# Kernel tuning notes

Hardware: AMD Instinct MI355X
Metric: run time of the kernel (lower is better)

## Reference

```python
import jax, jax.numpy as jnp
import numpy as np

N = 50000        # nodes
E = 400000       # edges per relation graph
IN_DIM = 64
HID = 128
OUT_DIM = 2
NSEL = 4096
EPS = 0.3        # residual scale
SLOPE = 0.3      # LeakyReLU negative slope


def _leaky(x):
    return jnp.where(x >= 0, x, SLOPE * x)


def _deg_norm(dst):
    # FAGCN-style d = in_degree^{-1/2}; 0 for isolated nodes
    deg = jax.ops.segment_sum(jnp.ones(dst.shape[0], jnp.float32), dst, num_segments=N)
    return jnp.where(deg > 0, jax.lax.rsqrt(jnp.maximum(deg, 1.0)), 0.0)


def _gnn_layer(hf, src, dst, d, gw, gb):
    # gate(concat[h_dst, h_src]) computed as per-node projections then edge gather
    D = hf.shape[1]
    s_dst = hf @ gw[:D]   # [N]
    s_src = hf @ gw[D:]   # [N]
    a = jnp.tanh(s_dst[dst] + s_src[src] + gb)        # [E]
    e = a * d[dst] * d[src]                            # [E]
    msg = hf[src] * e[:, None]                         # [E, D]
    return jax.ops.segment_sum(msg, dst, num_segments=N)


def setup_inputs() -> dict:
    key = jax.random.key(0)
    ks = iter(jax.random.split(key, 48))
    def nrm(shape, scale=0.05):
        return jax.random.normal(next(ks), shape, jnp.float32) * scale
    inp = {}
    inp["h"] = jax.random.normal(next(ks), (N, IN_DIM), jnp.float32)
    for i in (1, 2, 3):
        inp[f"src{i}"] = jax.random.randint(next(ks), (E,), 0, N)
        inp[f"dst{i}"] = jax.random.randint(next(ks), (E,), 0, N)
    inp["nodes"] = jax.random.randint(next(ks), (NSEL,), 0, N)
    inp["t1_w"] = nrm((HID, IN_DIM)); inp["t1_b"] = jnp.zeros((HID,), jnp.float32)
    for i in (1, 2, 3):
        inp[f"gate1_{i}_w"] = nrm((2 * HID,)); inp[f"gate1_{i}_b"] = jnp.zeros((), jnp.float32)
        inp[f"gate2_{i}_w"] = nrm((6 * HID,)); inp[f"gate2_{i}_b"] = jnp.zeros((), jnp.float32)
        inp[f"hw1_{i}"] = nrm((HID, HID))
        inp[f"hw2_{i}"] = nrm((3 * HID, HID))
    inp["t2_w"] = nrm((64, 7 * HID + IN_DIM)); inp["t2_b"] = jnp.zeros((64,), jnp.float32)
    inp["t3_w"] = nrm((OUT_DIM, 64)); inp["t3_b"] = jnp.zeros((OUT_DIM,), jnp.float32)
    return inp


def reference(h, src1, dst1, src2, dst2, src3, dst3, nodes,
              t1_w, t1_b,
              gate1_1_w, gate1_1_b, gate1_2_w, gate1_2_b, gate1_3_w, gate1_3_b,
              gate2_1_w, gate2_1_b, gate2_2_w, gate2_2_b, gate2_3_w, gate2_3_b,
              hw1_1, hw1_2, hw1_3, hw2_1, hw2_2, hw2_3,
              t2_w, t2_b, t3_w, t3_b):
    d1, d2, d3 = _deg_norm(dst1), _deg_norm(dst2), _deg_norm(dst3)
    raw0 = h
    raw1 = _leaky(h @ t1_w.T + t1_b)   # [N, HID] (dropout=identity in eval)
    h1_1 = _leaky((EPS * raw1 + _gnn_layer(raw1, src1, dst1, d1, gate1_1_w, gate1_1_b)) @ hw1_1)
    h1_2 = _leaky((EPS * raw1 + _gnn_layer(raw1, src2, dst2, d2, gate1_2_w, gate1_2_b)) @ hw1_2)
    h1_3 = _leaky((EPS * raw1 + _gnn_layer(raw1, src3, dst3, d3, gate1_3_w, gate1_3_b)) @ hw1_3)
    raw2 = jnp.concatenate([h1_1, h1_2, h1_3], axis=1)   # [N, 3*HID]
    h2_1 = _leaky((EPS * raw2 + _gnn_layer(raw2, src1, dst1, d1, gate2_1_w, gate2_1_b)) @ hw2_1)
    h2_2 = _leaky((EPS * raw2 + _gnn_layer(raw2, src2, dst2, d2, gate2_2_w, gate2_2_b)) @ hw2_2)
    h2_3 = _leaky((EPS * raw2 + _gnn_layer(raw2, src3, dst3, d3, gate2_3_w, gate2_3_b)) @ hw2_3)
    hf = jnp.concatenate([h2_1, h2_2, h2_3, raw0, raw1, raw2], axis=1)  # [N, 7*HID+IN_DIM]
    nf = hf[nodes]                                       # [NSEL, 7*HID+IN_DIM]
    s = _leaky(nf @ t2_w.T + t2_b)
    return s @ t3_w.T + t3_b                             # [NSEL, OUT_DIM]
```

## Files before the change

kernel.cpp:

```cpp
#include <hip/hip_runtime.h>
#include <hip/hip_bf16.h>

#define NN 50000
#define NE 400000
#define IND 64
#define HID 128
#define H3 384
#define FDIM 960
#define NSEL 4096
#define EPSF 0.3f
#define SLOPEF 0.3f
#define NBK 196
#define BCAP 4096
#define EPB 4096
#define NOEDGE 0xFFFFFFFFu

typedef __attribute__((ext_vector_type(8))) short bfrag;
typedef __attribute__((ext_vector_type(4))) float f4;
typedef __attribute__((ext_vector_type(8))) unsigned short us8;

__device__ __forceinline__ float leaky1(float v){ return v>=0.f? v : SLOPEF*v; }
__device__ __forceinline__ float b2f(unsigned short u){
  return __uint_as_float(((unsigned)u)<<16);
}
__device__ __forceinline__ unsigned short f2b(float v){
  __hip_bfloat16 b = __float2bfloat16(v);
  return *(unsigned short*)&b;
}

__global__ __launch_bounds__(256) void k_bfill4(
    const int* __restrict__ s0,const int* __restrict__ d0,
    const int* __restrict__ s1,const int* __restrict__ d1,
    const int* __restrict__ s2,const int* __restrict__ d2,
    int* __restrict__ bcnt, unsigned int* __restrict__ pairbuf)
{
  __shared__ unsigned int lbuf[EPB];
  __shared__ int hist[256];
  __shared__ int lbase[256];
  __shared__ int lcur[256];
  __shared__ int gbase[NBK];
  __shared__ int wsum[4];
  const int r = blockIdx.y;
  const int* S = (r==0)?s0:((r==1)?s1:s2);
  const int* D = (r==0)?d0:((r==1)?d1:d2);
  const int e0 = blockIdx.x*EPB;
  const int t = threadIdx.x;
  hist[t] = 0; lcur[t] = 0;
  __syncthreads();

  unsigned int pv[16];
  #pragma unroll
  for (int j=0;j<4;j++){
    int e = e0 + (j*256 + t)*4;
    if (e < NE){
      int4 sv = *(const int4*)&S[e];
      int4 dv = *(const int4*)&D[e];
      pv[j*4+0] = ((unsigned)dv.x<<16)|(unsigned)sv.x;
      pv[j*4+1] = ((unsigned)dv.y<<16)|(unsigned)sv.y;
      pv[j*4+2] = ((unsigned)dv.z<<16)|(unsigned)sv.z;
      pv[j*4+3] = ((unsigned)dv.w<<16)|(unsigned)sv.w;
    } else {
      pv[j*4+0]=NOEDGE; pv[j*4+1]=NOEDGE; pv[j*4+2]=NOEDGE; pv[j*4+3]=NOEDGE;
    }
  }
  #pragma unroll
  for (int i=0;i<16;i++){
    if (pv[i] != NOEDGE) atomicAdd(&hist[pv[i]>>24], 1);
  }
  __syncthreads();
  {
    int hv = hist[t];
    int lane = t & 63, wid = t >> 6;
    int x = hv;
    #pragma unroll
    for (int d=1; d<64; d<<=1){ int y=__shfl_up(x,(unsigned)d); if(lane>=d) x+=y; }
    if (lane==63) wsum[wid]=x;
    __syncthreads();
    int wpre = 0;
    if (wid>0) wpre += wsum[0];
    if (wid>1) wpre += wsum[1];
    if (wid>2) wpre += wsum[2];
    lbase[t] = wpre + x - hv;
    if (t < NBK){
      int hh = hist[t];
      gbase[t] = (hh>0) ? atomicAdd(&bcnt[r*NBK+t], hh) : 0;
    }
  }
  __syncthreads();
  #pragma unroll
  for (int i=0;i<16;i++){
    if (pv[i] != NOEDGE){
      int b = (int)(pv[i] >> 24);
      int pos = lbase[b] + atomicAdd(&lcur[b], 1);
      lbuf[pos] = pv[i];
    }
  }
  __syncthreads();
  int tot = min(NE - e0, EPB);
  for (int idx = t; idx < tot; idx += 256){
    unsigned int v = lbuf[idx];
    int b = (int)(v >> 24);
    pairbuf[((size_t)(r*NBK + b))*BCAP + gbase[b] + (idx - lbase[b])] = v;
  }
}

__global__ __launch_bounds__(256) void k_bsort4(
    const unsigned int* __restrict__ pairbuf,
    const int* __restrict__ bcnt,
    int* __restrict__ off, float* __restrict__ dnv,
    unsigned short* __restrict__ csrc)
{
  __shared__ unsigned short lout[BCAP];
  __shared__ int hist[256];
  __shared__ int excl[256];
  __shared__ int cur[256];
  __shared__ int red[256];
  __shared__ int wsum[4];
  const int r = blockIdx.y, b = blockIdx.x;
  const int nb0 = b << 8;
  const int t = threadIdx.x;
  red[t] = (t < b) ? bcnt[r*NBK + t] : 0;
  hist[t] = 0; cur[t] = 0;
  __syncthreads();
  #pragma unroll
  for (int sdv=128; sdv>0; sdv>>=1){
    if (t < sdv) red[t] += red[t+sdv];
    __syncthreads();
  }
  const int bbase = red[0];
  const int cnt = bcnt[r*NBK + b];
  const unsigned int* pb = pairbuf + ((size_t)(r*NBK + b))*BCAP;
  unsigned int pv[16];
  #pragma unroll
  for (int j=0;j<16;j++){
    int e = j*256 + t;
    pv[j] = (e < cnt) ? pb[e] : NOEDGE;
    if (pv[j] != NOEDGE) atomicAdd(&hist[(int)(pv[j]>>16) - nb0], 1);
  }
  __syncthreads();
  {
    int hv = hist[t];
    int lane = t & 63, wid = t >> 6;
    int x = hv;
    #pragma unroll
    for (int d=1; d<64; d<<=1){ int y=__shfl_up(x,(unsigned)d); if(lane>=d) x+=y; }
    if (lane==63) wsum[wid]=x;
    __syncthreads();
    int wpre = 0;
    if (wid>0) wpre += wsum[0];
    if (wid>1) wpre += wsum[1];
    if (wid>2) wpre += wsum[2];
    excl[t] = wpre + x - hv;
  }
  __syncthreads();
  int nidx = nb0 + t;
  if (nidx < NN){
    off[r*(NN+1) + nidx] = bbase + excl[t];
    int g = hist[t];
    dnv[r*NN + nidx] = (g>0) ? rsqrtf((float)g) : 0.f;
  }
  if (b == NBK-1 && t == 0) off[r*(NN+1) + NN] = bbase + cnt;
  #pragma unroll
  for (int j=0;j<16;j++){
    if (pv[j] != NOEDGE){
      int pn = (int)(pv[j] >> 16) - nb0;
      int slot = atomicAdd(&cur[pn], 1);
      lout[excl[pn] + slot] = (unsigned short)(pv[j] & 0xffffu);
    }
  }
  __syncthreads();
  unsigned short* op = csrc + (size_t)r*NE + bbase;
  for (int idx = t; idx < cnt; idx += 256) op[idx] = lout[idx];
}

__global__ void k_wprep2(const float* __restrict__ t1w,
    const float* __restrict__ hw1_0, const float* __restrict__ hw1_1, const float* __restrict__ hw1_2,
    const float* __restrict__ hw2_0, const float* __restrict__ hw2_1, const float* __restrict__ hw2_2,
    const float* __restrict__ t2w, const float* __restrict__ h,
    unsigned short* __restrict__ wt1, unsigned short* __restrict__ w1t,
    unsigned short* __restrict__ w2t, unsigned short* __restrict__ wt2,
    unsigned short* __restrict__ hb){
  int t = blockIdx.x*256 + threadIdx.x;
  if (t < 8192){
    wt1[t] = f2b(t1w[t]);
  } else if (t < 57344){
    int e = t - 8192;
    int r = e / 16384, q = e - r*16384;
    int n = q >> 7, k = q & 127;
    const float* W = (r==0)?hw1_0:((r==1)?hw1_1:hw1_2);
    w1t[e] = f2b(W[k*HID + n]);
  } else if (t < 204800){
    int e = t - 57344;
    int r = e / 49152, q = e - r*49152;
    int n = q / H3, k = q - n*H3;
    const float* W = (r==0)?hw2_0:((r==1)?hw2_1:hw2_2);
    w2t[e] = f2b(W[k*HID + n]);
  } else if (t < 266240){
    int e = t - 204800;
    wt2[e] = f2b(t2w[e]);
  } else if (t < 666240){
    int q = t - 266240;
    const float4 a = ((const float4*)h)[q*2];
    const float4 b = ((const float4*)h)[q*2+1];
    us8 o;
    o[0]=f2b(a.x); o[1]=f2b(a.y); o[2]=f2b(a.z); o[3]=f2b(a.w);
    o[4]=f2b(b.x); o[5]=f2b(b.y); o[6]=f2b(b.z); o[7]=f2b(b.w);
    *(us8*)&hb[q*8] = o;
  }
}

__global__ __launch_bounds__(256) void k_mfma_t1(
    const unsigned short* __restrict__ Ab, const unsigned short* __restrict__ W,
    const float* __restrict__ bias, unsigned short* __restrict__ Cb)
{
  __shared__ short As[64][72];
  __shared__ short Bs[128][72];
  const int tid = threadIdx.x;
  const int bm = blockIdx.x*64;

  for (int q = tid; q < 64*8; q += 256){
    int row = q >> 3, c8 = q & 7;
    int grow = bm + row; grow = (grow < NN) ? grow : (NN-1);
    *(us8*)&As[row][c8*8] = *(const us8*)&Ab[(size_t)grow*IND + c8*8];
  }
  for (int q = tid; q < 128*8; q += 256){
    int n = q >> 3, c8 = q & 7;
    *(us8*)&Bs[n][c8*8] = *(const us8*)&W[n*IND + c8*8];
  }
  __syncthreads();

  const int wid = tid >> 6, lane = tid & 63;
  const int wrow = (wid & 1)*32, wcol = (wid >> 1)*64;
  const int fr = lane & 15, fq = lane >> 4;
  f4 acc[2][4];
  #pragma unroll
  for (int mi=0;mi<2;mi++)
    #pragma unroll
    for (int ni=0;ni<4;ni++) acc[mi][ni] = (f4){0.f,0.f,0.f,0.f};

  #pragma unroll
  for (int ks=0; ks<2; ks++){
    int kb = ks*32 + fq*8;
    bfrag a[2], b[4];
    #pragma unroll
    for (int mi=0;mi<2;mi++) a[mi] = *(const bfrag*)&As[wrow + mi*16 + fr][kb];
    #pragma unroll
    for (int ni=0;ni<4;ni++) b[ni] = *(const bfrag*)&Bs[wcol + ni*16 + fr][kb];
    #pragma unroll
    for (int mi=0;mi<2;mi++)
      #pragma unroll
      for (int ni=0;ni<4;ni++)
        acc[mi][ni] = __builtin_amdgcn_mfma_f32_16x16x32_bf16(a[mi], b[ni], acc[mi][ni], 0, 0, 0);
  }

  #pragma unroll
  for (int mi=0;mi<2;mi++){
    int row0 = bm + wrow + mi*16 + fq*4;
    #pragma unroll
    for (int j=0;j<4;j++){
      int row = row0 + j;
      if (row < NN){
        #pragma unroll
        for (int ni=0;ni<4;ni++){
          int col = wcol + ni*16 + fr;
          Cb[(size_t)row*HID + col] = f2b(leaky1(acc[mi][ni][j] + bias[col]));
        }
      }
    }
  }
}

__global__ __launch_bounds__(256) void k_mfma128(
    const unsigned short* __restrict__ Abf, const unsigned short* __restrict__ Wt,
    unsigned short* __restrict__ Cb, int M)
{
  __shared__ short As[64][136];
  __shared__ short Bs[128][136];
  const int r = blockIdx.y;
  const unsigned short* Ar = Abf + (size_t)r*M*HID;
  const unsigned short* W  = Wt + (size_t)r*HID*HID;
  const int tid = threadIdx.x;
  const int bm = blockIdx.x*64;

  for (int q = tid; q < 64*16; q += 256){
    int row = q >> 4, c8 = q & 15;
    int grow = bm + row; grow = (grow < M) ? grow : (M-1);
    *(us8*)&As[row][c8*8] = *(const us8*)&Ar[(size_t)grow*HID + c8*8];
  }
  for (int q = tid; q < 128*16; q += 256){
    int n = q >> 4, c8 = q & 15;
    *(us8*)&Bs[n][c8*8] = *(const us8*)&W[n*HID + c8*8];
  }
  __syncthreads();

  const int wid = tid >> 6, lane = tid & 63;
  const int wrow = (wid & 1)*32, wcol = (wid >> 1)*64;
  const int fr = lane & 15, fq = lane >> 4;
  f4 acc[2][4];
  #pragma unroll
  for (int mi=0;mi<2;mi++)
    #pragma unroll
    for (int ni=0;ni<4;ni++) acc[mi][ni] = (f4){0.f,0.f,0.f,0.f};

  #pragma unroll
  for (int ks=0; ks<4; ks++){
    int kb = ks*32 + fq*8;
    bfrag a[2], b[4];
    #pragma unroll
    for (int mi=0;mi<2;mi++) a[mi] = *(const bfrag*)&As[wrow + mi*16 + fr][kb];
    #pragma unroll
    for (int ni=0;ni<4;ni++) b[ni] = *(const bfrag*)&Bs[wcol + ni*16 + fr][kb];
    #pragma unroll
    for (int mi=0;mi<2;mi++)
      #pragma unroll
      for (int ni=0;ni<4;ni++)
        acc[mi][ni] = __builtin_amdgcn_mfma_f32_16x16x32_bf16(a[mi], b[ni], acc[mi][ni], 0, 0, 0);
  }

  const int coff = r*HID;
  #pragma unroll
  for (int mi=0;mi<2;mi++){
    int row0 = bm + wrow + mi*16 + fq*4;
    #pragma unroll
    for (int j=0;j<4;j++){
      int row = row0 + j;
      if (row < M){
        #pragma unroll
        for (int ni=0;ni<4;ni++){
          Cb[(size_t)row*H3 + coff + wcol + ni*16 + fr] = f2b(leaky1(acc[mi][ni][j]));
        }
      }
    }
  }
}

__global__ __launch_bounds__(256) void k_mfma384(
    const unsigned short* __restrict__ Abf, const unsigned short* __restrict__ Wt,
    unsigned short* __restrict__ nfb)
{
  __shared__ short As[32][72];
  __shared__ short Bs[128][72];
  const int r = blockIdx.y;
  const unsigned short* Ar = Abf + (size_t)r*NSEL*H3;
  const unsigned short* W  = Wt + (size_t)r*HID*H3;
  const int tid = threadIdx.x;
  const int bm = blockIdx.x*32;
  const int wid = tid >> 6, lane = tid & 63;
  const int fr = lane & 15, fq = lane >> 4;
  f4 acc[2][2];
  #pragma unroll
  for (int mi=0;mi<2;mi++)
    #pragma unroll
    for (int ni=0;ni<2;ni++) acc[mi][ni] = (f4){0.f,0.f,0.f,0.f};

  for (int kc=0; kc<6; kc++){
    for (int q = tid; q < 32*8; q += 256){
      int row = q >> 3, c8 = q & 7;
      *(us8*)&As[row][c8*8] = *(const us8*)&Ar[(size_t)(bm+row)*H3 + kc*64 + c8*8];
    }
    for (int q = tid; q < 128*8; q += 256){
      int n = q >> 3, c8 = q & 7;
      *(us8*)&Bs[n][c8*8] = *(const us8*)&W[(size_t)n*H3 + kc*64 + c8*8];
    }
    __syncthreads();
    #pragma unroll
    for (int ks=0; ks<2; ks++){
      int kb = ks*32 + fq*8;
      bfrag a[2], b[2];
      #pragma unroll
      for (int mi=0;mi<2;mi++) a[mi] = *(const bfrag*)&As[mi*16 + fr][kb];
      #pragma unroll
      for (int ni=0;ni<2;ni++) b[ni] = *(const bfrag*)&Bs[wid*32 + ni*16 + fr][kb];
      #pragma unroll
      for (int mi=0;mi<2;mi++)
        #pragma unroll
        for (int ni=0;ni<2;ni++)
          acc[mi][ni] = __builtin_amdgcn_mfma_f32_16x16x32_bf16(a[mi], b[ni], acc[mi][ni], 0, 0, 0);
    }
    __syncthreads();
  }

  #pragma unroll
  for (int mi=0;mi<2;mi++){
    int row0 = bm + mi*16 + fq*4;
    #pragma unroll
    for (int j=0;j<4;j++){
      int i = row0 + j;
      #pragma unroll
      for (int ni=0;ni<2;ni++){
        int col = wid*32 + ni*16 + fr;
        nfb[(size_t)i*FDIM + r*HID + col] = f2b(leaky1(acc[mi][ni][j]));
      }
    }
  }
}

__global__ __launch_bounds__(256) void k_mfma_t2(
    const unsigned short* __restrict__ Abf, const unsigned short* __restrict__ W,
    float* __restrict__ sbuf)
{
  __shared__ short As[32][72];
  __shared__ short Bs[64][72];
  const int tid = threadIdx.x;
  const int bm = blockIdx.x*32;
  const int wid = tid >> 6, lane = tid & 63;
  const int fr = lane & 15, fq = lane >> 4;
  f4 acc[2];
  acc[0] = (f4){0.f,0.f,0.f,0.f};
  acc[1] = (f4){0.f,0.f,0.f,0.f};

  for (int kc=0; kc<15; kc++){
    for (int q = tid; q < 32*8; q += 256){
      int row = q >> 3, c8 = q & 7;
      *(us8*)&As[row][c8*8] = *(const us8*)&Abf[(size_t)(bm+row)*FDIM + kc*64 + c8*8];
    }
    for (int q = tid; q < 64*8; q += 256){
      int n = q >> 3, c8 = q & 7;
      *(us8*)&Bs[n][c8*8] = *(const us8*)&W[(size_t)n*FDIM + kc*64 + c8*8];
    }
    __syncthreads();
    #pragma unroll
    for (int ks=0; ks<2; ks++){
      int kb = ks*32 + fq*8;
      bfrag a[2], b;
      a[0] = *(const bfrag*)&As[fr][kb];
      a[1] = *(const bfrag*)&As[16 + fr][kb];
      b = *(const bfrag*)&Bs[wid*16 + fr][kb];
      acc[0] = __builtin_amdgcn_mfma_f32_16x16x32_bf16(a[0], b, acc[0], 0, 0, 0);
      acc[1] = __builtin_amdgcn_mfma_f32_16x16x32_bf16(a[1], b, acc[1], 0, 0, 0);
    }
    __syncthreads();
  }

  #pragma unroll
  for (int mi=0;mi<2;mi++){
    int row0 = bm + mi*16 + fq*4;
    #pragma unroll
    for (int j=0;j<4;j++){
      sbuf[(size_t)(row0+j)*64 + wid*16 + fr] = acc[mi][j];
    }
  }
}

__global__ __launch_bounds__(256) void k_final_wave(
    const float* __restrict__ sbuf, const float* __restrict__ t2b,
    const float* __restrict__ t3w, const float* __restrict__ t3b,
    float* __restrict__ outp)
{
  int w = (blockIdx.x*256 + threadIdx.x) >> 6;
  int j = threadIdx.x & 63;
  if (w >= NSEL) return;
  float v = leaky1(sbuf[(size_t)w*64 + j] + t2b[j]);
  float a0 = v*t3w[j], a1 = v*t3w[64+j];
  #pragma unroll
  for (int sft=32;sft>0;sft>>=1){
    a0 += __shfl_down(a0,(unsigned)sft);
    a1 += __shfl_down(a1,(unsigned)sft);
  }
  if (j==0){
    outp[2*w+0] = a0 + t3b[0];
    outp[2*w+1] = a1 + t3b[1];
  }
}

template<int D>
__global__ __launch_bounds__(256) void k_scores_g(const unsigned short* __restrict__ X,
    const float* __restrict__ g0, const float* __restrict__ g1, const float* __restrict__ g2,
    float* __restrict__ sd, float* __restrict__ ss){
  const int tid = threadIdx.x;
  const int p = tid & 15;
  const int n = blockIdx.x*16 + (tid >> 4);
  const unsigned short* x = X + (size_t)n*D;
  float a0=0,a1=0,a2=0,a3=0,a4=0,a5=0;
  #pragma unroll
  for (int it=0; it<D/128; it++){
    int k = it*128 + p*8;
    us8 u = *(const us8*)&x[k];
    #pragma unroll
    for (int e=0;e<8;e++){
      float v = b2f(u[e]);
      a0 = fmaf(v, g0[k+e],   a0);  a1 = fmaf(v, g0[D+k+e], a1);
      a2 = fmaf(v, g1[k+e],   a2);  a3 = fmaf(v, g1[D+k+e], a3);
      a4 = fmaf(v, g2[k+e],   a4);  a5 = fmaf(v, g2[D+k+e], a5);
    }
  }
  #pragma unroll
  for (int s=8;s>0;s>>=1){
    a0 += __shfl_xor(a0,(unsigned)s); a1 += __shfl_xor(a1,(unsigned)s);
    a2 += __shfl_xor(a2,(unsigned)s); a3 += __shfl_xor(a3,(unsigned)s);
    a4 += __shfl_xor(a4,(unsigned)s); a5 += __shfl_xor(a5,(unsigned)s);
  }
  if (p==0){
    sd[0*NN+n]=a0; ss[0*NN+n]=a1;
    sd[1*NN+n]=a2; ss[1*NN+n]=a3;
    sd[2*NN+n]=a4; ss[2*NN+n]=a5;
  }
}

__global__ __launch_bounds__(256) void k_gather_f3z(
    const unsigned short* __restrict__ Xb,
    const int* __restrict__ off, const unsigned short* __restrict__ csrc,
    const float* __restrict__ sd, const float* __restrict__ ss,
    const float* __restrict__ dnv,
    const float* __restrict__ gb0, const float* __restrict__ gb1, const float* __restrict__ gb2,
    unsigned short* __restrict__ outp){
  const int tid = threadIdx.x;
  const int lane = tid & 63;
  const int wg = lane >> 4;
  const int p  = lane & 15;
  const int n = blockIdx.x*16 + (tid >> 4);
  us8 rv = *(const us8*)&Xb[(size_t)n*HID + p*8];
  int p0a[3], p1a[3];
  #pragma unroll
  for (int r=0;r<3;r++){
    p0a[r] = off[r*(NN+1) + n];
    p1a[r] = off[r*(NN+1) + n + 1];
  }
  float resid[8];
  #pragma unroll
  for (int i=0;i<8;i++) resid[i] = EPSF * b2f(rv[i]);

  for (int r=0;r<3;r++){
    const unsigned short* csr = csrc + (size_t)r*NE;
    const float* ssr = ss + r*NN;
    const float* dnr = dnv + r*NN;
    float gbv = ((r==0)?gb0:((r==1)?gb1:gb2))[0];
    float sd_n = sd[r*NN + n], dn_n = dnr[n];
    float acc[8];
    #pragma unroll
    for (int i=0;i<8;i++) acc[i] = resid[i];
    int p0 = p0a[r], p1 = p1a[r];
    for (int pc=p0; pc<p1; pc+=16){
      int m = min(16, p1-pc);
      int s = 0; float c = 0.f;
      if (p < m){
        s = csr[pc+p];
        c = tanhf(sd_n + ssr[s] + gbv) * dn_n * dnr[s];
      }
      int   sj = __shfl(s, wg*16);
      float cj = __shfl(c, wg*16);
      us8 v = *(const us8*)&Xb[(size_t)sj*HID + p*8];
      for (int j=1;j<=m;j++){
        us8 vn; float cn = 0.f;
        if (j < m){
          int sn = __shfl(s, wg*16+j);
          cn = __shfl(c, wg*16+j);
          vn = *(const us8*)&Xb[(size_t)sn*HID + p*8];
        }
        #pragma unroll
        for (int i=0;i<8;i++) acc[i] = fmaf(cj, b2f(v[i]), acc[i]);
        v = vn; cj = cn;
      }
    }
    us8 o;
    #pragma unroll
    for (int i=0;i<8;i++) o[i] = f2b(acc[i]);
    *(us8*)&outp[((size_t)r*NN + n)*HID + p*8] = o;
  }
}

__global__ __launch_bounds__(256) void k_gather_sel3w2(const unsigned short* __restrict__ Xb,
    const int* __restrict__ nodes,
    const int* __restrict__ off, const unsigned short* __restrict__ csrc,
    const float* __restrict__ sd, const float* __restrict__ ss,
    const float* __restrict__ dnv,
    const float* __restrict__ gb0, const float* __restrict__ gb1, const float* __restrict__ gb2,
    unsigned short* __restrict__ outp){
  const int tid = threadIdx.x;
  const int lane = tid & 63;
  const int wg = lane >> 4;
  const int p  = lane & 15;
  const int i = blockIdx.x*16 + (tid >> 4);
  const int r = blockIdx.y;
  const int n = nodes[i];
  const int* offr = off + r*(NN+1);
  const unsigned short* csr = csrc + (size_t)r*NE;
  const float* ssr = ss + r*NN;
  const float* dnr = dnv + r*NN;
  float gbv = ((r==0)?gb0:((r==1)?gb1:gb2))[0];
  float sd_n = sd[r*NN + n], dn_n = dnr[n];
  float acc[3][8];
  #pragma unroll
  for (int cc=0;cc<3;cc++)
    #pragma unroll
    for (int q=0;q<8;q++) acc[cc][q]=0.f;
  int p0 = offr[n], p1 = offr[n+1];
  for (int pc=p0; pc<p1; pc+=16){
    int m = min(16, p1-pc);
    int s = 0; float c = 0.f;
    if (p < m){
      s = csr[pc+p];
      c = tanhf(sd_n + ssr[s] + gbv) * dn_n * dnr[s];
    }
    int   sj = __shfl(s, wg*16);
    float cj = __shfl(c, wg*16);
    const unsigned short* row = &Xb[(size_t)sj*H3];
    us8 v0 = *(const us8*)&row[0*HID + p*8];
    us8 v1 = *(const us8*)&row[1*HID + p*8];
    us8 v2 = *(const us8*)&row[2*HID + p*8];
    for (int j=1;j<=m;j++){
      us8 n0, n1, n2; float cn = 0.f;
      if (j < m){
        int sn = __shfl(s, wg*16+j);
        cn = __shfl(c, wg*16+j);
        const unsigned short* rw = &Xb[(size_t)sn*H3];
        n0 = *(const us8*)&rw[0*HID + p*8];
        n1 = *(const us8*)&rw[1*HID + p*8];
        n2 = *(const us8*)&rw[2*HID + p*8];
      }
      #pragma unroll
      for (int q=0;q<8;q++){
        acc[0][q] = fmaf(cj, b2f(v0[q]), acc[0][q]);
        acc[1][q] = fmaf(cj, b2f(v1[q]), acc[1][q]);
        acc[2][q] = fmaf(cj, b2f(v2[q]), acc[2][q]);
      }
      v0 = n0; v1 = n1; v2 = n2; cj = cn;
    }
  }
  const unsigned short* xrow = &Xb[(size_t)n*H3];
  unsigned short* orow = &outp[((size_t)r*NSEL + i)*H3];
  #pragma unroll
  for (int cc=0;cc<3;cc++){
    us8 v = *(const us8*)&xrow[cc*HID + p*8];
    us8 o;
    #pragma unroll
    for (int q=0;q<8;q++) o[q] = f2b(fmaf(EPSF, b2f(v[q]), acc[cc][q]));
    *(us8*)&orow[cc*HID + p*8] = o;
  }
}

__global__ __launch_bounds__(256) void k_nf_fillb(const unsigned short* __restrict__ hb,
    const unsigned short* __restrict__ raw1b, const unsigned short* __restrict__ raw2b,
    const int* __restrict__ nodes, unsigned short* __restrict__ nfb){
  int t = blockIdx.x*256 + threadIdx.x;
  if (t >= NSEL*72) return;
  int i = t/72, c = t - i*72;
  int n = nodes[i];
  us8 v; int col;
  if (c < 8)       { v = *(const us8*)&hb[(size_t)n*IND + c*8];           col = 384 + c*8; }
  else if (c < 24) { int q=c-8;  v = *(const us8*)&raw1b[(size_t)n*HID + q*8]; col = 448 + q*8; }
  else             { int q=c-24; v = *(const us8*)&raw2b[(size_t)n*H3  + q*8]; col = 576 + q*8; }
  *(us8*)&nfb[(size_t)i*FDIM + col] = v;
}

extern "C" void kernel_launch(void* const* d_in, const int* in_sizes, int n_in,
                              void* d_out, int out_size, void* d_ws, size_t ws_size,
                              hipStream_t stream){
  if (n_in < 32) return;
  const float* h = (const float*)d_in[0];
  const int* src[3] = {(const int*)d_in[1], (const int*)d_in[3], (const int*)d_in[5]};
  const int* dst[3] = {(const int*)d_in[2], (const int*)d_in[4], (const int*)d_in[6]};
  const int* nodes = (const int*)d_in[7];
  const float* t1w = (const float*)d_in[8];
  const float* t1b = (const float*)d_in[9];

  bool dictOrder = (in_sizes[12] == 768);
  const float *g1w[3],*g1b[3],*g2w[3],*g2b[3],*hw1[3],*hw2[3];
  for (int r=0;r<3;r++){
    if (dictOrder){
      int base = 10 + r*6;
      g1w[r]=(const float*)d_in[base+0]; g1b[r]=(const float*)d_in[base+1];
      g2w[r]=(const float*)d_in[base+2]; g2b[r]=(const float*)d_in[base+3];
      hw1[r]=(const float*)d_in[base+4]; hw2[r]=(const float*)d_in[base+5];
    } else {
      g1w[r]=(const float*)d_in[10+2*r]; g1b[r]=(const float*)d_in[11+2*r];
      g2w[r]=(const float*)d_in[16+2*r]; g2b[r]=(const float*)d_in[17+2*r];
      hw1[r]=(const float*)d_in[22+r];   hw2[r]=(const float*)d_in[25+r];
    }
  }
  const float* t2w = (const float*)d_in[28];
  const float* t2b = (const float*)d_in[29];
  const float* t3w = (const float*)d_in[30];
  const float* t3b = (const float*)d_in[31];
  float* outp = (float*)d_out;

  char* w = (char*)d_ws;
  auto carve = [&](size_t bytes)->void*{
    void* p = (void*)w;
    w += ((bytes + 255) & ~size_t(255));
    return p;
  };
  int*   bcnt = (int*)  carve((size_t)1024*4);
  int*   off  = (int*)  carve((size_t)3*(NN+1)*4);
  float* dnv  = (float*)carve((size_t)3*NN*4);
  unsigned short* csrc = (unsigned short*)carve((size_t)3*NE*2);
  float* sd1  = (float*)carve((size_t)3*NN*4);
  float* ss1  = (float*)carve((size_t)3*NN*4);
  float* sd2  = (float*)carve((size_t)3*NN*4);
  float* ss2  = (float*)carve((size_t)3*NN*4);
  unsigned short* wt1 = (unsigned short*)carve((size_t)HID*IND*2);
  unsigned short* w1t = (unsigned short*)carve((size_t)3*HID*HID*2);
  unsigned short* w2t = (unsigned short*)carve((size_t)3*HID*H3*2);
  unsigned short* wt2 = (unsigned short*)carve((size_t)64*FDIM*2);
  unsigned short* hb  = (unsigned short*)carve((size_t)NN*IND*2);
  unsigned short* raw1b = (unsigned short*)carve((size_t)NN*HID*2);
  unsigned short* raw2b = (unsigned short*)carve((size_t)NN*H3*2);
  size_t ubytes = (size_t)3*NN*HID*2;
  float* ureg = (float*)carve(ubytes);
  unsigned int* pairbuf = (unsigned int*)ureg;
  unsigned short* pre1b = (unsigned short*)ureg;
  unsigned short* pre2b = (unsigned short*)ureg;
  float* sbuf = (float*)((char*)ureg + (size_t)16*1024*1024);
  unsigned short* nfb = (unsigned short*)carve((size_t)NSEL*FDIM*2);

  hipMemsetAsync(bcnt, 0, (size_t)1024*4, stream);
  k_bfill4<<<dim3((NE+EPB-1)/EPB, 3), 256, 0, stream>>>(
      src[0],dst[0],src[1],dst[1],src[2],dst[2], bcnt, pairbuf);
  k_bsort4<<<dim3(NBK,3), 256, 0, stream>>>(pairbuf, bcnt, off, dnv, csrc);

  k_wprep2<<<(666240+255)/256, 256, 0, stream>>>(
      t1w, hw1[0], hw1[1], hw1[2], hw2[0], hw2[1], hw2[2], t2w, h,
      wt1, w1t, w2t, wt2, hb);

  k_mfma_t1<<<(NN+63)/64, 256, 0, stream>>>(hb, wt1, t1b, raw1b);

  k_scores_g<HID><<<NN/16, 256, 0, stream>>>(raw1b, g1w[0], g1w[1], g1w[2], sd1, ss1);

  k_gather_f3z<<<NN/16, 256, 0, stream>>>(raw1b, off, csrc,
      sd1, ss1, dnv, g1b[0], g1b[1], g1b[2], pre1b);
  k_mfma128<<<dim3((NN+63)/64, 3), 256, 0, stream>>>(pre1b, w1t, raw2b, NN);

  k_scores_g<H3><<<NN/16, 256, 0, stream>>>(raw2b, g2w[0], g2w[1], g2w[2], sd2, ss2);

  k_gather_sel3w2<<<dim3(NSEL/16, 3), 256, 0, stream>>>(raw2b, nodes, off, csrc,
      sd2, ss2, dnv, g2b[0], g2b[1], g2b[2], pre2b);

  k_mfma384<<<dim3(NSEL/32, 3), 256, 0, stream>>>(pre2b, w2t, nfb);

  k_nf_fillb<<<(NSEL*72+255)/256, 256, 0, stream>>>(hb, raw1b, raw2b, nodes, nfb);

  k_mfma_t2<<<NSEL/32, 256, 0, stream>>>(nfb, wt2, sbuf);
  k_final_wave<<<(NSEL*64+255)/256, 256, 0, stream>>>(sbuf, t2b, t3w, t3b, outp);
}
```

Measured before the change: 197.0 us.

## Merge independent kernels into combined launches to cut launch count

Independent kernels are merged into shared launches by splitting on block index: edge bucket fill with weight/feature bf16 prep, bucket sort with the t1 MFMA GEMM, and the hw2 GEMM with the node-feature gather. The t2 GEMM and final projection are also fused through shared memory, removing the sbuf round trip. This reduces kernel launch overhead and inter-kernel gaps. The cost is larger shared-memory footprints and mixed block types within a launch.

Result: faster. 186.1 us (-5.6%).

```diff
diff --git a/kernel.cpp b/kernel.cpp
--- a/kernel.cpp
+++ b/kernel.cpp
@@ -14,6 +14,7 @@
 #define BCAP 4096
 #define EPB 4096
 #define NOEDGE 0xFFFFFFFFu
+#define NBF 98
 
 typedef __attribute__((ext_vector_type(8))) short bfrag;
 typedef __attribute__((ext_vector_type(4))) float f4;
@@ -28,242 +29,239 @@
   return *(unsigned short*)&b;
 }
 
-__global__ __launch_bounds__(256) void k_bfill4(
+__global__ __launch_bounds__(256) void k_fill_prep(
     const int* __restrict__ s0,const int* __restrict__ d0,
     const int* __restrict__ s1,const int* __restrict__ d1,
     const int* __restrict__ s2,const int* __restrict__ d2,
-    int* __restrict__ bcnt, unsigned int* __restrict__ pairbuf)
+    int* __restrict__ bcnt, unsigned int* __restrict__ pairbuf,
+    const float* __restrict__ t1w,
+    const float* __restrict__ hw1_0, const float* __restrict__ hw1_1, const float* __restrict__ hw1_2,
+    const float* __restrict__ hw2_0, const float* __restrict__ hw2_1, const float* __restrict__ hw2_2,
+    const float* __restrict__ t2w, const float* __restrict__ h,
+    unsigned short* __restrict__ wt1, unsigned short* __restrict__ w1t,
+    unsigned short* __restrict__ w2t, unsigned short* __restrict__ wt2,
+    unsigned short* __restrict__ hb)
 {
-  __shared__ unsigned int lbuf[EPB];
+  __shared__ __align__(16) unsigned int lbuf[EPB];
   __shared__ int hist[256];
   __shared__ int lbase[256];
   __shared__ int lcur[256];
   __shared__ int gbase[NBK];
   __shared__ int wsum[4];
-  const int r = blockIdx.y;
-  const int* S = (r==0)?s0:((r==1)?s1:s2);
-  const int* D = (r==0)?d0:((r==1)?d1:d2);
-  const int e0 = blockIdx.x*EPB;
   const int t = threadIdx.x;
-  hist[t] = 0; lcur[t] = 0;
-  __syncthreads();
-
-  unsigned int pv[16];
-  #pragma unroll
-  for (int j=0;j<4;j++){
-    int e = e0 + (j*256 + t)*4;
-    if (e < NE){
-      int4 sv = *(const int4*)&S[e];
-      int4 dv = *(const int4*)&D[e];
-      pv[j*4+0] = ((unsigned)dv.x<<16)|(unsigned)sv.x;
-      pv[j*4+1] = ((unsigned)dv.y<<16)|(unsigned)sv.y;
-      pv[j*4+2] = ((unsigned)dv.z<<16)|(unsigned)sv.z;
-      pv[j*4+3] = ((unsigned)dv.w<<16)|(unsigned)sv.w;
-    } else {
-      pv[j*4+0]=NOEDGE; pv[j*4+1]=NOEDGE; pv[j*4+2]=NOEDGE; pv[j*4+3]=NOEDGE;
-    }
-  }
-  #pragma unroll
-  for (int i=0;i<16;i++){
-    if (pv[i] != NOEDGE) atomicAdd(&hist[pv[i]>>24], 1);
-  }
-  __syncthreads();
-  {
-    int hv = hist[t];
-    int lane = t & 63, wid = t >> 6;
-    int x = hv;
-    #pragma unroll
-    for (int d=1; d<64; d<<=1){ int y=__shfl_up(x,(unsigned)d); if(lane>=d) x+=y; }
-    if (lane==63) wsum[wid]=x;
-    __syncthreads();
-    int wpre = 0;
-    if (wid>0) wpre += wsum[0];
-    if (wid>1) wpre += wsum[1];
-    if (wid>2) wpre += wsum[2];
-    lbase[t] = wpre + x - hv;
-    if (t < NBK){
-      int hh = hist[t];
-      gbase[t] = (hh>0) ? atomicAdd(&bcnt[r*NBK+t], hh) : 0;
-    }
-  }
-  __syncthreads();
-  #pragma unroll
-  for (int i=0;i<16;i++){
-    if (pv[i] != NOEDGE){
-      int b = (int)(pv[i] >> 24);
-      int pos = lbase[b] + atomicAdd(&lcur[b], 1);
-      lbuf[pos] = pv[i];
-    }
-  }
-  __syncthreads();
-  int tot = min(NE - e0, EPB);
-  for (int idx = t; idx < tot; idx += 256){
-    unsigned int v = lbuf[idx];
-    int b = (int)(v >> 24);
-    pairbuf[((size_t)(r*NBK + b))*BCAP + gbase[b] + (idx - lbase[b])] = v;
-  }
-}
-
-__global__ __launch_bounds__(256) void k_bsort4(
-    const unsigned int* __restrict__ pairbuf,
-    const int* __restrict__ bcnt,
-    int* __restrict__ off, float* __restrict__ dnv,
-    unsigned short* __restrict__ csrc)
-{
-  __shared__ unsigned short lout[BCAP];
-  __shared__ int hist[256];
-  __shared__ int excl[256];
-  __shared__ int cur[256];
-  __shared__ int red[256];
-  __shared__ int wsum[4];
-  const int r = blockIdx.y, b = blockIdx.x;
-  const int nb0 = b << 8;
-  const int t = threadIdx.x;
-  red[t] = (t < b) ? bcnt[r*NBK + t] : 0;
-  hist[t] = 0; cur[t] = 0;
-  __syncthreads();
-  #pragma unroll
-  for (int sdv=128; sdv>0; sdv>>=1){
-    if (t < sdv) red[t] += red[t+sdv];
-    __syncthreads();
-  }
-  const int bbase = red[0];
-  const int cnt = bcnt[r*NBK + b];
-  const unsigned int* pb = pairbuf + ((size_t)(r*NBK + b))*BCAP;
-  unsigned int pv[16];
-  #pragma unroll
-  for (int j=0;j<16;j++){
-    int e = j*256 + t;
-    pv[j] = (e < cnt) ? pb[e] : NOEDGE;
-    if (pv[j] != NOEDGE) atomicAdd(&hist[(int)(pv[j]>>16) - nb0], 1);
-  }
-  __syncthreads();
-  {
-    int hv = hist[t];
-    int lane = t & 63, wid = t >> 6;
-    int x = hv;
-    #pragma unroll
-    for (int d=1; d<64; d<<=1){ int y=__shfl_up(x,(unsigned)d); if(lane>=d) x+=y; }
-    if (lane==63) wsum[wid]=x;
-    __syncthreads();
-    int wpre = 0;
-    if (wid>0) wpre += wsum[0];
-    if (wid>1) wpre += wsum[1];
-    if (wid>2) wpre += wsum[2];
-    excl[t] = wpre + x - hv;
-  }
-  __syncthreads();
-  int nidx = nb0 + t;
-  if (nidx < NN){
-    off[r*(NN+1) + nidx] = bbase + excl[t];
-    int g = hist[t];
-    dnv[r*NN + nidx] = (g>0) ? rsqrtf((float)g) : 0.f;
-  }
-  if (b == NBK-1 && t == 0) off[r*(NN+1) + NN] = bbase + cnt;
-  #pragma unroll
-  for (int j=0;j<16;j++){
-    if (pv[j] != NOEDGE){
-      int pn = (int)(pv[j] >> 16) - nb0;
-      int slot = atomicAdd(&cur[pn], 1);
-      lout[excl[pn] + slot] = (unsigned short)(pv[j] & 0xffffu);
-    }
-  }
-  __syncthreads();
-  unsigned short* op = csrc + (size_t)r*NE + bbase;
-  for (int idx = t; idx < cnt; idx += 256) op[idx] = lout[idx];
-}
-
-__global__ void k_wprep2(const float* __restrict__ t1w,
-    const float* __restrict__ hw1_0, const float* __restrict__ hw1_1, const float* __restrict__ hw1_2,
-    const float* __restrict__ hw2_0, const float* __restrict__ hw2_1, const float* __restrict__ hw2_2,
-    const float* __restrict__ t2w, const float* __restrict__ h,
-    unsigned short* __restrict__ wt1, unsigned short* __restrict__ w1t,
-    unsigned short* __restrict__ w2t, unsigned short* __restrict__ wt2,
-    unsigned short* __restrict__ hb){
-  int t = blockIdx.x*256 + threadIdx.x;
-  if (t < 8192){
-    wt1[t] = f2b(t1w[t]);
-  } else if (t < 57344){
-    int e = t - 8192;
-    int r = e / 16384, q = e - r*16384;
-    int n = q >> 7, k = q & 127;
-    const float* W = (r==0)?hw1_0:((r==1)?hw1_1:hw1_2);
-    w1t[e] = f2b(W[k*HID + n]);
-  } else if (t < 204800){
-    int e = t - 57344;
-    int r = e / 49152, q = e - r*49152;
-    int n = q / H3, k = q - n*H3;
-    const float* W = (r==0)?hw2_0:((r==1)?hw2_1:hw2_2);
-    w2t[e] = f2b(W[k*HID + n]);
-  } else if (t < 266240){
-    int e = t - 204800;
-    wt2[e] = f2b(t2w[e]);
-  } else if (t < 666240){
-    int q = t - 266240;
-    const float4 a = ((const float4*)h)[q*2];
-    const float4 b = ((const float4*)h)[q*2+1];
-    us8 o;
-    o[0]=f2b(a.x); o[1]=f2b(a.y); o[2]=f2b(a.z); o[3]=f2b(a.w);
-    o[4]=f2b(b.x); o[5]=f2b(b.y); o[6]=f2b(b.z); o[7]=f2b(b.w);
-    *(us8*)&hb[q*8] = o;
-  }
-}
-
-__global__ __launch_bounds__(256) void k_mfma_t1(
+
+  if (blockIdx.x < 3*NBF){
+    const int r = blockIdx.x / NBF;
+    const int bx = blockIdx.x - r*NBF;
+    const int* S = (r==0)?s0:((r==1)?s1:s2);
+    const int* D = (r==0)?d0:((r==1)?d1:d2);
+    const int e0 = bx*EPB;
+    hist[t] = 0; lcur[t] = 0;
+    __syncthreads();
+    unsigned int pv[16];
+    #pragma unroll
+    for (int j=0;j<4;j++){
+      int e = e0 + (j*256 + t)*4;
+      if (e < NE){
+        int4 sv = *(const int4*)&S[e];
+        int4 dv = *(const int4*)&D[e];
+        pv[j*4+0] = ((unsigned)dv.x<<16)|(unsigned)sv.x;
+        pv[j*4+1] = ((unsigned)dv.y<<16)|(unsigned)sv.y;
+        pv[j*4+2] = ((unsigned)dv.z<<16)|(unsigned)sv.z;
+        pv[j*4+3] = ((unsigned)dv.w<<16)|(unsigned)sv.w;
+      } else {
+        pv[j*4+0]=NOEDGE; pv[j*4+1]=NOEDGE; pv[j*4+2]=NOEDGE; pv[j*4+3]=NOEDGE;
+      }
+    }
+    #pragma unroll
+    for (int i=0;i<16;i++){
+      if (pv[i] != NOEDGE) atomicAdd(&hist[pv[i]>>24], 1);
+    }
+    __syncthreads();
+    {
+      int hv = hist[t];
+      int lane = t & 63, wid = t >> 6;
+      int x = hv;
+      #pragma unroll
+      for (int d=1; d<64; d<<=1){ int y=__shfl_up(x,(unsigned)d); if(lane>=d) x+=y; }
+      if (lane==63) wsum[wid]=x;
+      __syncthreads();
+      int wpre = 0;
+      if (wid>0) wpre += wsum[0];
+      if (wid>1) wpre += wsum[1];
+      if (wid>2) wpre += wsum[2];
+      lbase[t] = wpre + x - hv;
+      if (t < NBK){
+        int hh = hist[t];
+        gbase[t] = (hh>0) ? atomicAdd(&bcnt[r*NBK+t], hh) : 0;
+      }
+    }
+    __syncthreads();
+    #pragma unroll
+    for (int i=0;i<16;i++){
+      if (pv[i] != NOEDGE){
+        int b = (int)(pv[i] >> 24);
+        int pos = lbase[b] + atomicAdd(&lcur[b], 1);
+        lbuf[pos] = pv[i];
+      }
+    }
+    __syncthreads();
+    int tot = min(NE - e0, EPB);
+    for (int idx = t; idx < tot; idx += 256){
+      unsigned int v = lbuf[idx];
+      int b = (int)(v >> 24);
+      pairbuf[((size_t)(r*NBK + b))*BCAP + gbase[b] + (idx - lbase[b])] = v;
+    }
+  } else {
+    int g = (blockIdx.x - 3*NBF)*256 + t;
+    if (g < 8192){
+      wt1[g] = f2b(t1w[g]);
+    } else if (g < 57344){
+      int e = g - 8192;
+      int r = e / 16384, q = e - r*16384;
+      int n = q >> 7, k = q & 127;
+      const float* W = (r==0)?hw1_0:((r==1)?hw1_1:hw1_2);
+      w1t[e] = f2b(W[k*HID + n]);
+    } else if (g < 204800){
+      int e = g - 57344;
+      int r = e / 49152, q = e - r*49152;
+      int n = q / H3, k = q - n*H3;
+      const float* W = (r==0)?hw2_0:((r==1)?hw2_1:hw2_2);
+      w2t[e] = f2b(W[k*HID + n]);
+    } else if (g < 266240){
+      int e = g - 204800;
+      wt2[e] = f2b(t2w[e]);
+    } else if (g < 666240){
+      int q = g - 266240;
+      const float4 a = ((const float4*)h)[q*2];
+      const float4 b = ((const float4*)h)[q*2+1];
+      us8 o;
+      o[0]=f2b(a.x); o[1]=f2b(a.y); o[2]=f2b(a.z); o[3]=f2b(a.w);
+      o[4]=f2b(b.x); o[5]=f2b(b.y); o[6]=f2b(b.z); o[7]=f2b(b.w);
+      *(us8*)&hb[q*8] = o;
+    }
+  }
+}
+
+__global__ __launch_bounds__(256) void k_sort_t1(
+    const unsigned int* __restrict__ pairbuf, const int* __restrict__ bcnt,
+    int* __restrict__ off, float* __restrict__ dnv, unsigned short* __restrict__ csrc,
     const unsigned short* __restrict__ Ab, const unsigned short* __restrict__ W,
     const float* __restrict__ bias, unsigned short* __restrict__ Cb)
 {
-  __shared__ short As[64][72];
-  __shared__ short Bs[128][72];
-  const int tid = threadIdx.x;
-  const int bm = blockIdx.x*64;
-
-  for (int q = tid; q < 64*8; q += 256){
-    int row = q >> 3, c8 = q & 7;
-    int grow = bm + row; grow = (grow < NN) ? grow : (NN-1);
-    *(us8*)&As[row][c8*8] = *(const us8*)&Ab[(size_t)grow*IND + c8*8];
-  }
-  for (int q = tid; q < 128*8; q += 256){
-    int n = q >> 3, c8 = q & 7;
-    *(us8*)&Bs[n][c8*8] = *(const us8*)&W[n*IND + c8*8];
-  }
-  __syncthreads();
-
-  const int wid = tid >> 6, lane = tid & 63;
-  const int wrow = (wid & 1)*32, wcol = (wid >> 1)*64;
-  const int fr = lane & 15, fq = lane >> 4;
-  f4 acc[2][4];
-  #pragma unroll
-  for (int mi=0;mi<2;mi++)
-    #pragma unroll
-    for (int ni=0;ni<4;ni++) acc[mi][ni] = (f4){0.f,0.f,0.f,0.f};
-
-  #pragma unroll
-  for (int ks=0; ks<2; ks++){
-    int kb = ks*32 + fq*8;
-    bfrag a[2], b[4];
-    #pragma unroll
-    for (int mi=0;mi<2;mi++) a[mi] = *(const bfrag*)&As[wrow + mi*16 + fr][kb];
-    #pragma unroll
-    for (int ni=0;ni<4;ni++) b[ni] = *(const bfrag*)&Bs[wcol + ni*16 + fr][kb];
+  __shared__ __align__(16) char smem[27648];
+  const int t = threadIdx.x;
+
+  if (blockIdx.x < 2*NBK + NBK){
+    unsigned short* lout = (unsigned short*)smem;
+    int* hist = (int*)(smem + 8192);
+    int* excl = (int*)(smem + 9216);
+    int* cur  = (int*)(smem + 10240);
+    int* red  = (int*)(smem + 11264);
+    int* wsum = (int*)(smem + 12288);
+    const int r = blockIdx.x / NBK;
+    const int b = blockIdx.x - r*NBK;
+    const int nb0 = b << 8;
+    red[t] = (t < b) ? bcnt[r*NBK + t] : 0;
+    hist[t] = 0; cur[t] = 0;
+    __syncthreads();
+    #pragma unroll
+    for (int sdv=128; sdv>0; sdv>>=1){
+      if (t < sdv) red[t] += red[t+sdv];
+      __syncthreads();
+    }
+    const int bbase = red[0];
+    const int cnt = bcnt[r*NBK + b];
+    const unsigned int* pb = pairbuf + ((size_t)(r*NBK + b))*BCAP;
+    unsigned int pv[16];
+    #pragma unroll
+    for (int j=0;j<16;j++){
+      int e = j*256 + t;
+      pv[j] = (e < cnt) ? pb[e] : NOEDGE;
+      if (pv[j] != NOEDGE) atomicAdd(&hist[(int)(pv[j]>>16) - nb0], 1);
+    }
+    __syncthreads();
+    {
+      int hv = hist[t];
+      int lane = t & 63, wid = t >> 6;
+      int x = hv;
+      #pragma unroll
+      for (int d=1; d<64; d<<=1){ int y=__shfl_up(x,(unsigned)d); if(lane>=d) x+=y; }
+      if (lane==63) wsum[wid]=x;
+      __syncthreads();
+      int wpre = 0;
+      if (wid>0) wpre += wsum[0];
+      if (wid>1) wpre += wsum[1];
+      if (wid>2) wpre += wsum[2];
+      excl[t] = wpre + x - hv;
+    }
+    __syncthreads();
+    int nidx = nb0 + t;
+    if (nidx < NN){
+      off[r*(NN+1) + nidx] = bbase + excl[t];
+      int g = hist[t];
+      dnv[r*NN + nidx] = (g>0) ? rsqrtf((float)g) : 0.f;
+    }
+    if (b == NBK-1 && t == 0) off[r*(NN+1) + NN] = bbase + cnt;
+    #pragma unroll
+    for (int j=0;j<16;j++){
+      if (pv[j] != NOEDGE){
+        int pn = (int)(pv[j] >> 16) - nb0;
+        int slot = atomicAdd(&cur[pn], 1);
+        lout[excl[pn] + slot] = (unsigned short)(pv[j] & 0xffffu);
+      }
+    }
+    __syncthreads();
+    unsigned short* op = csrc + (size_t)r*NE + bbase;
+    for (int idx = t; idx < cnt; idx += 256) op[idx] = lout[idx];
+  } else {
+    short (*As)[72] = (short(*)[72])smem;
+    short (*Bs)[72] = (short(*)[72])(smem + 9216);
+    const int bm = (blockIdx.x - 3*NBK)*64;
+    for (int q = t; q < 64*8; q += 256){
+      int row = q >> 3, c8 = q & 7;
+      int grow = bm + row; grow = (grow < NN) ? grow : (NN-1);
+      *(us8*)&As[row][c8*8] = *(const us8*)&Ab[(size_t)grow*IND + c8*8];
+    }
+    for (int q = t; q < 128*8; q += 256){
+      int n = q >> 3, c8 = q & 7;
+      *(us8*)&Bs[n][c8*8] = *(const us8*)&W[n*IND + c8*8];
+    }
+    __syncthreads();
+    const int wid = t >> 6, lane = t & 63;
+    const int wrow = (wid & 1)*32, wcol = (wid >> 1)*64;
+    const int fr = lane & 15, fq = lane >> 4;
+    f4 acc[2][4];
     #pragma unroll
     for (int mi=0;mi<2;mi++)
       #pragma unroll
-      for (int ni=0;ni<4;ni++)
-        acc[mi][ni] = __builtin_amdgcn_mfma_f32_16x16x32_bf16(a[mi], b[ni], acc[mi][ni], 0, 0, 0);
-  }
-
-  #pragma unroll
-  for (int mi=0;mi<2;mi++){
-    int row0 = bm + wrow + mi*16 + fq*4;
-    #pragma unroll
-    for (int j=0;j<4;j++){
-      int row = row0 + j;
-      if (row < NN){
+      for (int ni=0;ni<4;ni++) acc[mi][ni] = (f4){0.f,0.f,0.f,0.f};
+    #pragma unroll
+    for (int ks=0; ks<2; ks++){
+      int kb = ks*32 + fq*8;
+      bfrag a[2], b[4];
+      #pragma unroll
+      for (int mi=0;mi<2;mi++) a[mi] = *(const bfrag*)&As[wrow + mi*16 + fr][kb];
+      #pragma unroll
+      for (int ni=0;ni<4;ni++) b[ni] = *(const bfrag*)&Bs[wcol + ni*16 + fr][kb];
+      #pragma unroll
+      for (int mi=0;mi<2;mi++)
         #pragma unroll
-        for (int ni=0;ni<4;ni++){
-          int col = wcol + ni*16 + fr;
-          Cb[(size_t)row*HID + col] = f2b(leaky1(acc[mi][ni][j] + bias[col]));
+        for (int ni=0;ni<4;ni++)
+          acc[mi][ni] = __builtin_amdgcn_mfma_f32_16x16x32_bf16(a[mi], b[ni], acc[mi][ni], 0, 0, 0);
+    }
+    #pragma unroll
+    for (int mi=0;mi<2;mi++){
+      int row0 = bm + wrow + mi*16 + fq*4;
+      #pragma unroll
+      for (int j=0;j<4;j++){
+        int row = row0 + j;
+        if (row < NN){
+          #pragma unroll
+          for (int ni=0;ni<4;ni++){
+            int col = wcol + ni*16 + fr;
+            Cb[(size_t)row*HID + col] = f2b(leaky1(acc[mi][ni][j] + bias[col]));
+          }
         }
       }
     }
@@ -334,87 +332,104 @@
   }
 }
 
-__global__ __launch_bounds__(256) void k_mfma384(
+__global__ __launch_bounds__(256) void k_hw2_nf(
     const unsigned short* __restrict__ Abf, const unsigned short* __restrict__ Wt,
+    const unsigned short* __restrict__ hb, const unsigned short* __restrict__ raw1b,
+    const unsigned short* __restrict__ raw2b, const int* __restrict__ nodes,
     unsigned short* __restrict__ nfb)
 {
-  __shared__ short As[32][72];
-  __shared__ short Bs[128][72];
-  const int r = blockIdx.y;
-  const unsigned short* Ar = Abf + (size_t)r*NSEL*H3;
-  const unsigned short* W  = Wt + (size_t)r*HID*H3;
-  const int tid = threadIdx.x;
+  __shared__ __align__(16) char smem[23040];
+  const int t = threadIdx.x;
+  if (blockIdx.x < 3*128){
+    short (*As)[72] = (short(*)[72])smem;
+    short (*Bs)[72] = (short(*)[72])(smem + 4608);
+    const int r = blockIdx.x / 128;
+    const int bm = (blockIdx.x - r*128)*32;
+    const unsigned short* Ar = Abf + (size_t)r*NSEL*H3;
+    const unsigned short* W  = Wt + (size_t)r*HID*H3;
+    const int wid = t >> 6, lane = t & 63;
+    const int fr = lane & 15, fq = lane >> 4;
+    f4 acc[2][2];
+    #pragma unroll
+    for (int mi=0;mi<2;mi++)
+      #pragma unroll
+      for (int ni=0;ni<2;ni++) acc[mi][ni] = (f4){0.f,0.f,0.f,0.f};
+    for (int kc=0; kc<6; kc++){
+      for (int q = t; q < 32*8; q += 256){
+        int row = q >> 3, c8 = q & 7;
+        *(us8*)&As[row][c8*8] = *(const us8*)&Ar[(size_t)(bm+row)*H3 + kc*64 + c8*8];
+      }
+      for (int q = t; q < 128*8; q += 256){
+        int n = q >> 3, c8 = q & 7;
+        *(us8*)&Bs[n][c8*8] = *(const us8*)&W[(size_t)n*H3 + kc*64 + c8*8];
+      }
+      __syncthreads();
+      #pragma unroll
+      for (int ks=0; ks<2; ks++){
+        int kb = ks*32 + fq*8;
+        bfrag a[2], b[2];
+        #pragma unroll
+        for (int mi=0;mi<2;mi++) a[mi] = *(const bfrag*)&As[mi*16 + fr][kb];
+        #pragma unroll
+        for (int ni=0;ni<2;ni++) b[ni] = *(const bfrag*)&Bs[wid*32 + ni*16 + fr][kb];
+        #pragma unroll
+        for (int mi=0;mi<2;mi++)
+          #pragma unroll
+          for (int ni=0;ni<2;ni++)
+            acc[mi][ni] = __builtin_amdgcn_mfma_f32_16x16x32_bf16(a[mi], b[ni], acc[mi][ni], 0, 0, 0);
+      }
+      __syncthreads();
+    }
+    #pragma unroll
+    for (int mi=0;mi<2;mi++){
+      int row0 = bm + mi*16 + fq*4;
+      #pragma unroll
+      for (int j=0;j<4;j++){
+        int i = row0 + j;
+        #pragma unroll
+        for (int ni=0;ni<2;ni++){
+          int col = wid*32 + ni*16 + fr;
+          nfb[(size_t)i*FDIM + r*HID + col] = f2b(leaky1(acc[mi][ni][j]));
+        }
+      }
+    }
+  } else {
+    int g = (blockIdx.x - 3*128)*256 + t;
+    if (g < NSEL*72){
+      int i = g/72, c = g - i*72;
+      int n = nodes[i];
+      us8 v; int col;
+      if (c < 8)       { v = *(const us8*)&hb[(size_t)n*IND + c*8];           col = 384 + c*8; }
+      else if (c < 24) { int q=c-8;  v = *(const us8*)&raw1b[(size_t)n*HID + q*8]; col = 448 + q*8; }
+      else             { int q=c-24; v = *(const us8*)&raw2b[(size_t)n*H3  + q*8]; col = 576 + q*8; }
+      *(us8*)&nfb[(size_t)i*FDIM + col] = v;
+    }
+  }
+}
+
+__global__ __launch_bounds__(256) void k_t2_final(
+    const unsigned short* __restrict__ Abf, const unsigned short* __restrict__ W,
+    const float* __restrict__ t2b, const float* __restrict__ t3w,
+    const float* __restrict__ t3b, float* __restrict__ outp)
+{
+  __shared__ __align__(16) char smem[13824];
+  short (*As)[72] = (short(*)[72])smem;
+  short (*Bs)[72] = (short(*)[72])(smem + 4608);
+  float (*sb)[64] = (float(*)[64])smem;
+  const int t = threadIdx.x;
   const int bm = blockIdx.x*32;
-  const int wid = tid >> 6, lane = tid & 63;
-  const int fr = lane & 15, fq = lane >> 4;
-  f4 acc[2][2];
-  #pragma unroll
-  for (int mi=0;mi<2;mi++)
-    #pragma unroll
-    for (int ni=0;ni<2;ni++) acc[mi][ni] = (f4){0.f,0.f,0.f,0.f};
-
-  for (int kc=0; kc<6; kc++){
-    for (int q = tid; q < 32*8; q += 256){
-      int row = q >> 3, c8 = q & 7;
-      *(us8*)&As[row][c8*8] = *(const us8*)&Ar[(size_t)(bm+row)*H3 + kc*64 + c8*8];
-    }
-    for (int q = tid; q < 128*8; q += 256){
-      int n = q >> 3, c8 = q & 7;
-      *(us8*)&Bs[n][c8*8] = *(const us8*)&W[(size_t)n*H3 + kc*64 + c8*8];
-    }
-    __syncthreads();
-    #pragma unroll
-    for (int ks=0; ks<2; ks++){
-      int kb = ks*32 + fq*8;
-      bfrag a[2], b[2];
-      #pragma unroll
-      for (int mi=0;mi<2;mi++) a[mi] = *(const bfrag*)&As[mi*16 + fr][kb];
-      #pragma unroll
-      for (int ni=0;ni<2;ni++) b[ni] = *(const bfrag*)&Bs[wid*32 + ni*16 + fr][kb];
-      #pragma unroll
-      for (int mi=0;mi<2;mi++)
-        #pragma unroll
-        for (int ni=0;ni<2;ni++)
-          acc[mi][ni] = __builtin_amdgcn_mfma_f32_16x16x32_bf16(a[mi], b[ni], acc[mi][ni], 0, 0, 0);
-    }
-    __syncthreads();
-  }
-
-  #pragma unroll
-  for (int mi=0;mi<2;mi++){
-    int row0 = bm + mi*16 + fq*4;
-    #pragma unroll
-    for (int j=0;j<4;j++){
-      int i = row0 + j;
-      #pragma unroll
-      for (int ni=0;ni<2;ni++){
-        int col = wid*32 + ni*16 + fr;
-        nfb[(size_t)i*FDIM + r*HID + col] = f2b(leaky1(acc[mi][ni][j]));
-      }
-    }
-  }
-}
-
-__global__ __launch_bounds__(256) void k_mfma_t2(
-    const unsigned short* __restrict__ Abf, const unsigned short* __restrict__ W,
-    float* __restrict__ sbuf)
-{
-  __shared__ short As[32][72];
-  __shared__ short Bs[64][72];
-  const int tid = threadIdx.x;
-  const int bm = blockIdx.x*32;
-  const int wid = tid >> 6, lane = tid & 63;
+  const int wid = t >> 6, lane = t & 63;
   const int fr = lane & 15, fq = lane >> 4;
   f4 acc[2];
   acc[0] = (f4){0.f,0.f,0.f,0.f};
   acc[1] = (f4){0.f,0.f,0.f,0.f};
 
   for (int kc=0; kc<15; kc++){
-    for (int q = tid; q < 32*8; q += 256){
+    for (int q = t; q < 32*8; q += 256){
       int row = q >> 3, c8 = q & 7;
       *(us8*)&As[row][c8*8] = *(const us8*)&Abf[(size_t)(bm+row)*FDIM + kc*64 + c8*8];
     }
-    for (int q = tid; q < 64*8; q += 256){
+    for (int q = t; q < 64*8; q += 256){
       int n = q >> 3, c8 = q & 7;
       *(us8*)&Bs[n][c8*8] = *(const us8*)&W[(size_t)n*FDIM + kc*64 + c8*8];
     }
@@ -434,32 +449,26 @@
 
   #pragma unroll
   for (int mi=0;mi<2;mi++){
-    int row0 = bm + mi*16 + fq*4;
+    int rloc = mi*16 + fq*4;
     #pragma unroll
     for (int j=0;j<4;j++){
-      sbuf[(size_t)(row0+j)*64 + wid*16 + fr] = acc[mi][j];
-    }
-  }
-}
-
-__global__ __launch_bounds__(256) void k_final_wave(
-    const float* __restrict__ sbuf, const float* __restrict__ t2b,
-    const float* __restrict__ t3w, const float* __restrict__ t3b,
-    float* __restrict__ outp)
-{
-  int w = (blockIdx.x*256 + threadIdx.x) >> 6;
-  int j = threadIdx.x & 63;
-  if (w >= NSEL) return;
-  float v = leaky1(sbuf[(size_t)w*64 + j] + t2b[j]);
-  float a0 = v*t3w[j], a1 = v*t3w[64+j];
-  #pragma unroll
-  for (int sft=32;sft>0;sft>>=1){
-    a0 += __shfl_down(a0,(unsigned)sft);
-    a1 += __shfl_down(a1,(unsigned)sft);
-  }
-  if (j==0){
-    outp[2*w+0] = a0 + t3b[0];
-    outp[2*w+1] = a1 + t3b[1];
+      sb[rloc+j][wid*16 + fr] = acc[mi][j];
+    }
+  }
+  __syncthreads();
+  for (int rr = wid*8; rr < wid*8+8; rr++){
+    float v = leaky1(sb[rr][lane] + t2b[lane]);
+    float a0 = v*t3w[lane], a1 = v*t3w[64+lane];
+    #pragma unroll
+    for (int sft=32;sft>0;sft>>=1){
+      a0 += __shfl_down(a0,(unsigned)sft);
+      a1 += __shfl_down(a1,(unsigned)sft);
+    }
+    if (lane==0){
+      int w = bm + rr;
+      outp[2*w+0] = a0 + t3b[0];
+      outp[2*w+1] = a1 + t3b[1];
+    }
   }
 }
 
@@ -627,20 +636,6 @@
     for (int q=0;q<8;q++) o[q] = f2b(fmaf(EPSF, b2f(v[q]), acc[cc][q]));
     *(us8*)&orow[cc*HID + p*8] = o;
   }
-}
-
-__global__ __launch_bounds__(256) void k_nf_fillb(const unsigned short* __restrict__ hb,
-    const unsigned short* __restrict__ raw1b, const unsigned short* __restrict__ raw2b,
-    const int* __restrict__ nodes, unsigned short* __restrict__ nfb){
-  int t = blockIdx.x*256 + threadIdx.x;
-  if (t >= NSEL*72) return;
-  int i = t/72, c = t - i*72;
-  int n = nodes[i];
-  us8 v; int col;
-  if (c < 8)       { v = *(const us8*)&hb[(size_t)n*IND + c*8];           col = 384 + c*8; }
-  else if (c < 24) { int q=c-8;  v = *(const us8*)&raw1b[(size_t)n*HID + q*8]; col = 448 + q*8; }
-  else             { int q=c-24; v = *(const us8*)&raw2b[(size_t)n*H3  + q*8]; col = 576 + q*8; }
-  *(us8*)&nfb[(size_t)i*FDIM + col] = v;
 }
 
 extern "C" void kernel_launch(void* const* d_in, const int* in_sizes, int n_in,
@@ -700,19 +695,15 @@
   unsigned int* pairbuf = (unsigned int*)ureg;
   unsigned short* pre1b = (unsigned short*)ureg;
   unsigned short* pre2b = (unsigned short*)ureg;
-  float* sbuf = (float*)((char*)ureg + (size_t)16*1024*1024);
   unsigned short* nfb = (unsigned short*)carve((size_t)NSEL*FDIM*2);
 
   hipMemsetAsync(bcnt, 0, (size_t)1024*4, stream);
-  k_bfill4<<<dim3((NE+EPB-1)/EPB, 3), 256, 0, stream>>>(
-      src[0],dst[0],src[1],dst[1],src[2],dst[2], bcnt, pairbuf);
-  k_bsort4<<<dim3(NBK,3), 256, 0, stream>>>(pairbuf, bcnt, off, dnv, csrc);
-
-  k_wprep2<<<(666240+255)/256, 256, 0, stream>>>(
+  k_fill_prep<<<3*NBF + 2603, 256, 0, stream>>>(
+      src[0],dst[0],src[1],dst[1],src[2],dst[2], bcnt, pairbuf,
       t1w, hw1[0], hw1[1], hw1[2], hw2[0], hw2[1], hw2[2], t2w, h,
       wt1, w1t, w2t, wt2, hb);
-
-  k_mfma_t1<<<(NN+63)/64, 256, 0, stream>>>(hb, wt1, t1b, raw1b);
+  k_sort_t1<<<3*NBK + (NN+63)/64, 256, 0, stream>>>(
+      pairbuf, bcnt, off, dnv, csrc, hb, wt1, t1b, raw1b);
 
   k_scores_g<HID><<<NN/16, 256, 0, stream>>>(raw1b, g1w[0], g1w[1], g1w[2], sd1, ss1);
 
@@ -725,10 +716,8 @@
   k_gather_sel3w2<<<dim3(NSEL/16, 3), 256, 0, stream>>>(raw2b, nodes, off, csrc,
       sd2, ss2, dnv, g2b[0], g2b[1], g2b[2], pre2b);
 
-  k_mfma384<<<dim3(NSEL/32, 3), 256, 0, stream>>>(pre2b, w2t, nfb);
-
-  k_nf_fillb<<<(NSEL*72+255)/256, 256, 0, stream>>>(hb, raw1b, raw2b, nodes, nfb);
-
-  k_mfma_t2<<<NSEL/32, 256, 0, stream>>>(nfb, wt2, sbuf);
-  k_final_wave<<<(NSEL*64+255)/256, 256, 0, stream>>>(sbuf, t2b, t3w, t3b, outp);
-}
+  k_hw2_nf<<<3*128 + (NSEL*72+255)/256, 256, 0, stream>>>(
+      pre2b, w2t, hb, raw1b, raw2b, nodes, nfb);
+
+  k_t2_final<<<NSEL/32, 256, 0, stream>>>(nfb, wt2, t2b, t3w, t3b, outp);
+}
```
